# Kernel tuning notes

Hardware: AMD Instinct MI355X
Metric: run time of the kernel (lower is better)

## Reference

```python
import jax, jax.numpy as jnp
import numpy as np

N_NODES = 100000
N_EDGES = 1000000
N_GRAPHS = 16
D_NODE = 64
D_EDGE = 32
D_GLOB = 32
OUT_DIM = 64
IN1 = 2 * D_NODE + D_EDGE + D_GLOB  # 192
IN2 = D_NODE + OUT_DIM + D_GLOB     # 160


def setup_inputs() -> dict:
    key = jax.random.key(0)
    ks = jax.random.split(key, 9)
    x = jax.random.normal(ks[0], (N_NODES, D_NODE), dtype=jnp.float32)
    edge_index = jax.random.randint(ks[1], (2, N_EDGES), 0, N_NODES, dtype=jnp.int64 if jax.config.jax_enable_x64 else jnp.int32)
    edge_attr = jax.random.normal(ks[2], (N_EDGES, D_EDGE), dtype=jnp.float32)
    u = jax.random.normal(ks[3], (N_GRAPHS, D_GLOB), dtype=jnp.float32)
    batch = jnp.sort(jax.random.randint(ks[4], (N_NODES,), 0, N_GRAPHS))
    # Linear params (kaiming-ish scale)
    W1 = jax.random.normal(ks[5], (IN1, OUT_DIM), dtype=jnp.float32) / np.sqrt(IN1)
    b1 = jnp.zeros((OUT_DIM,), dtype=jnp.float32)
    W2 = jax.random.normal(ks[6], (IN2, OUT_DIM), dtype=jnp.float32) / np.sqrt(IN2)
    b2 = jnp.zeros((OUT_DIM,), dtype=jnp.float32)
    return {"x": x, "edge_index": edge_index, "edge_attr": edge_attr, "u": u,
            "batch": batch, "W1": W1, "b1": b1, "W2": W2, "b2": b2}


def reference(x, edge_index, edge_attr, u, batch, W1, b1, W2, b2):
    src = edge_index[0]  # [E]
    dst = edge_index[1]  # [E]
    u_per_node = u[batch]  # [N, Du] gather globals to nodes
    # gather-concat: [E, 2D + De + Du]
    all_feat = jnp.concatenate([x[dst], x[src], edge_attr, u_per_node[dst]], axis=-1)
    # mlp_1 + ReLU on every edge message
    msg = jax.nn.relu(all_feat @ W1 + b1)  # [E, out]
    # scatter-sum to destination nodes
    agg = jax.ops.segment_sum(msg, dst, num_segments=x.shape[0])  # [N, out]
    # mlp_2 + ReLU on nodes
    node_in = jnp.concatenate([x, agg, u_per_node], axis=-1)  # [N, D + out + Du]
    return jax.nn.relu(node_in @ W2 + b2)
```

## Files before the change

kernel.cpp:

```cpp
#include <hip/hip_runtime.h>

constexpr int N_NODES = 100000;
constexpr int N_EDGES = 1000000;
constexpr int D_NODE  = 64;
constexpr int D_EDGE  = 32;
constexpr int D_GLOB  = 32;
constexpr int OUT_DIM = 64;
constexpr int K1 = 2*D_NODE + D_EDGE + D_GLOB;
constexpr int K2 = D_NODE + OUT_DIM + D_GLOB;

typedef _Float16 f16x8 __attribute__((ext_vector_type(8)));
typedef unsigned short ushort8_t __attribute__((ext_vector_type(8)));
typedef float floatx16 __attribute__((ext_vector_type(16)));

constexpr int FS = 200;

constexpr size_t WS_W1T = 0;
constexpr size_t WS_W2T = 24576;
constexpr size_t WS_UB  = 45056;
constexpr size_t WS_XB  = 46080;

__device__ inline unsigned pack_f2(float a, float b) {
    auto h = __builtin_amdgcn_cvt_pkrtz(a, b);
    return __builtin_bit_cast(unsigned, h);
}

__global__ __launch_bounds__(256) void prep_kernel(
    const float* __restrict__ x, const float* __restrict__ u,
    const float* __restrict__ W1, const float* __restrict__ W2,
    unsigned short* __restrict__ ws_w1t, unsigned short* __restrict__ ws_w2t,
    unsigned short* __restrict__ ws_ub, unsigned short* __restrict__ ws_xb)
{
    const int t = blockIdx.x * 256 + threadIdx.x;
    const int stride = gridDim.x * 256;
    const float4* x4 = (const float4*)x;
    for (int i = t; i < N_NODES * 16; i += stride) {
        float4 v = x4[i];
        uint2 pk;
        pk.x = pack_f2(v.x, v.y);
        pk.y = pack_f2(v.z, v.w);
        *(uint2*)&ws_xb[i * 4] = pk;
    }
    for (int i = t; i < K1 * 64; i += stride) {
        int k = i >> 6, n = i & 63;
        _Float16 h = (_Float16)W1[i];
        ws_w1t[n * K1 + k] = __builtin_bit_cast(unsigned short, h);
    }
    for (int i = t; i < K2 * 64; i += stride) {
        int k = i >> 6, n = i & 63;
        _Float16 h = (_Float16)W2[i];
        ws_w2t[n * K2 + k] = __builtin_bit_cast(unsigned short, h);
    }
    for (int i = t; i < 16 * D_GLOB; i += stride) {
        _Float16 h = (_Float16)u[i];
        ws_ub[i] = __builtin_bit_cast(unsigned short, h);
    }
}

__global__ __launch_bounds__(256, 4) void edge_kernel(
    const unsigned short* __restrict__ xb, const int* __restrict__ ei,
    const float* __restrict__ ea, const unsigned short* __restrict__ ub,
    const int* __restrict__ batch, const unsigned short* __restrict__ W1t,
    const float* __restrict__ b1, float* __restrict__ out)
{
    __shared__ __align__(16) unsigned short smem[64 * FS];
    __shared__ int s_dst[64];
    __shared__ int s_src[64];
    __shared__ int s_b[64];

    const int tid  = threadIdx.x;
    const int lane = tid & 63;
    const int wv   = tid >> 6;
    const int tile = blockIdx.x;
    const int eh   = wv >> 1;
    const int nh   = wv & 1;
    const int col  = lane & 31;
    const int half = lane >> 5;

    if (tid < 64) {
        int e = tile * 64 + tid;
        int d = ei[N_EDGES + e];
        s_dst[tid] = d;
        s_src[tid] = ei[e];
        s_b[tid]   = batch[d];
    }

    f16x8 Wf[12];
    #pragma unroll
    for (int s = 0; s < 12; ++s)
        Wf[s] = __builtin_bit_cast(f16x8,
            *(const ushort8_t*)&W1t[(nh*32 + col) * K1 + s*16 + half*8]);

    const int chp = (lane & 31) * 2;
    const float2 bv = *(const float2*)&b1[chp];

    __syncthreads();

    const float4* ea4 = (const float4*)ea;
    for (int q = tid; q < 64 * 24; q += 256) {
        int el = q / 24;
        int c  = q - el * 24;
        uint4 pk;
        if (c < 8)       pk = *(const uint4*)&xb[s_dst[el] * 64 + c * 8];
        else if (c < 16) pk = *(const uint4*)&xb[s_src[el] * 64 + (c - 8) * 8];
        else if (c < 20) {
            float4 v0 = ea4[(tile*64 + el) * 8 + (c - 16) * 2 + 0];
            float4 v1 = ea4[(tile*64 + el) * 8 + (c - 16) * 2 + 1];
            pk.x = pack_f2(v0.x, v0.y); pk.y = pack_f2(v0.z, v0.w);
            pk.z = pack_f2(v1.x, v1.y); pk.w = pack_f2(v1.z, v1.w);
        } else           pk = *(const uint4*)&ub[s_b[el] * 32 + (c - 20) * 8];
        *(uint4*)&smem[el * FS + c * 8] = pk;
    }
    __syncthreads();

    floatx16 acc = {0,0,0,0,0,0,0,0,0,0,0,0,0,0,0,0};
    #pragma unroll
    for (int s = 0; s < 12; ++s) {
        f16x8 a = __builtin_bit_cast(f16x8,
            *(const ushort8_t*)&smem[(eh*32 + col) * FS + s*16 + half*8]);
        acc = __builtin_amdgcn_mfma_f32_32x32x16_f16(a, Wf[s], acc, 0, 0, 0);
    }

    __syncthreads();
    float* smemf = (float*)smem;
    #pragma unroll
    for (int r = 0; r < 16; ++r) {
        int e = eh*32 + (r & 3) + 8*(r >> 2) + 4*half;
        smemf[e * 64 + nh*32 + col] = acc[r];
    }
    __syncthreads();

    #pragma unroll
    for (int it = 0; it < 8; ++it) {
        int e = wv*16 + it*2 + half;
        float2 m = *(const float2*)&smemf[e * 64 + chp];
        float v0 = m.x + bv.x; v0 = v0 > 0.f ? v0 : 0.f;
        float v1 = m.y + bv.y; v1 = v1 > 0.f ? v1 : 0.f;
        unsigned pk = pack_f2(v0, v1);
        unsigned short* p = (unsigned short*)out + (size_t)s_dst[e] * 128 + chp;
        asm volatile("global_atomic_pk_add_f16 %0, %1, off"
                     :: "v"(p), "v"(pk) : "memory");
    }
}

__global__ __launch_bounds__(256, 4) void node_kernel(
    const unsigned short* __restrict__ xb, const unsigned short* __restrict__ ub,
    const int* __restrict__ batch, const unsigned short* __restrict__ W2t,
    const float* __restrict__ b2, float* __restrict__ out)
{
    __shared__ __align__(16) unsigned short smem[64 * FS];
    __shared__ int s_b[64];

    const int tid  = threadIdx.x;
    const int lane = tid & 63;
    const int wv   = tid >> 6;
    const int base = blockIdx.x * 64;
    const int eh   = wv >> 1;
    const int nh   = wv & 1;
    const int col  = lane & 31;
    const int half = lane >> 5;

    if (tid < 64) {
        int n = base + tid;
        s_b[tid] = (n < N_NODES) ? batch[n] : 0;
    }

    f16x8 Bf[10];
    #pragma unroll
    for (int s = 0; s < 10; ++s)
        Bf[s] = __builtin_bit_cast(f16x8,
            *(const ushort8_t*)&W2t[(nh*32 + col) * K2 + s*16 + half*8]);
    const float b2v = b2[nh*32 + col];

    __syncthreads();

    const unsigned short* aggb = (const unsigned short*)out;
    for (int q = tid; q < 64 * 20; q += 256) {
        int nl = q / 20;
        int c  = q - nl * 20;
        int n  = base + nl;
        uint4 pk;
        if (n >= N_NODES) pk = uint4{0, 0, 0, 0};
        else if (c < 8)   pk = *(const uint4*)&xb[n * 64 + c * 8];
        else if (c < 16)  pk = *(const uint4*)&aggb[(size_t)n * 128 + (c - 8) * 8];
        else              pk = *(const uint4*)&ub[s_b[nl] * 32 + (c - 16) * 8];
        *(uint4*)&smem[nl * FS + c * 8] = pk;
    }
    __syncthreads();

    floatx16 acc = {0,0,0,0,0,0,0,0,0,0,0,0,0,0,0,0};
    #pragma unroll
    for (int s = 0; s < 10; ++s) {
        f16x8 a = __builtin_bit_cast(f16x8,
            *(const ushort8_t*)&smem[(eh*32 + col) * FS + s*16 + half*8]);
        acc = __builtin_amdgcn_mfma_f32_32x32x16_f16(a, Bf[s], acc, 0, 0, 0);
    }

    #pragma unroll
    for (int r = 0; r < 16; ++r) {
        int n = base + eh*32 + (r & 3) + 8*(r >> 2) + 4*half;
        if (n < N_NODES) {
            float vv = acc[r] + b2v;
            out[n * 64 + nh*32 + col] = vv > 0.f ? vv : 0.f;
        }
    }
}

extern "C" void kernel_launch(void* const* d_in, const int* in_sizes, int n_in,
                              void* d_out, int out_size, void* d_ws, size_t ws_size,
                              hipStream_t stream) {
    const float* x     = (const float*)d_in[0];
    const int*   ei    = (const int*)d_in[1];
    const float* ea    = (const float*)d_in[2];
    const float* u     = (const float*)d_in[3];
    const int*   batch = (const int*)d_in[4];
    const float* W1    = (const float*)d_in[5];
    const float* b1    = (const float*)d_in[6];
    const float* W2    = (const float*)d_in[7];
    const float* b2    = (const float*)d_in[8];
    float* out = (float*)d_out;

    unsigned short* ws_w1t = (unsigned short*)((char*)d_ws + WS_W1T);
    unsigned short* ws_w2t = (unsigned short*)((char*)d_ws + WS_W2T);
    unsigned short* ws_ub  = (unsigned short*)((char*)d_ws + WS_UB);
    unsigned short* ws_xb  = (unsigned short*)((char*)d_ws + WS_XB);

    (void)hipMemsetAsync(out, 0, (size_t)out_size * sizeof(float), stream);

    prep_kernel<<<2048, 256, 0, stream>>>(x, u, W1, W2, ws_w1t, ws_w2t, ws_ub, ws_xb);
    edge_kernel<<<N_EDGES / 64, 256, 0, stream>>>(ws_xb, ei, ea, ws_ub, batch, ws_w1t, b1, out);
    node_kernel<<<(N_NODES + 63) / 64, 256, 0, stream>>>(ws_xb, ws_ub, batch, ws_w2t, b2, out);
}
```

Baseline: 437.3 us.

## Sort edges by destination and pre-reduce messages before atomic scatter

Adds a counting sort of edges by destination node (histogram, two-level prefix scan, atomic scatter into a permutation), and the edge kernel now processes edges in sorted order. Within each 16-edge run the epilogue accumulates consecutive same-destination messages in registers before issuing the packed f16 atomic, reducing atomic traffic. It also raises launch-bound occupancy hints to 6. The cost is extra kernels and passes over edge_index, plus gathers of edge_attr that are no longer contiguous. With about 10 edges per node on average, the runs of equal destinations inside 16-edge groups are short.

```diff
diff --git a/kernel.cpp b/kernel.cpp
--- a/kernel.cpp
+++ b/kernel.cpp
@@ -15,10 +15,14 @@
 
 constexpr int FS = 200;
 
-constexpr size_t WS_W1T = 0;
-constexpr size_t WS_W2T = 24576;
-constexpr size_t WS_UB  = 45056;
-constexpr size_t WS_XB  = 46080;
+constexpr size_t WS_W1T  = 0;
+constexpr size_t WS_W2T  = 24576;
+constexpr size_t WS_UB   = 45056;
+constexpr size_t WS_XB   = 46080;
+constexpr size_t WS_CNT  = 12846080;
+constexpr size_t WS_CUR  = 13370368;
+constexpr size_t WS_SORT = 13894656;
+constexpr int BSUM_BASE  = 130048;
 
 __device__ inline unsigned pack_f2(float a, float b) {
     auto h = __builtin_amdgcn_cvt_pkrtz(a, b);
@@ -28,6 +32,7 @@
 __global__ __launch_bounds__(256) void prep_kernel(
     const float* __restrict__ x, const float* __restrict__ u,
     const float* __restrict__ W1, const float* __restrict__ W2,
+    const int* __restrict__ ei, int* __restrict__ cnt,
     unsigned short* __restrict__ ws_w1t, unsigned short* __restrict__ ws_w2t,
     unsigned short* __restrict__ ws_ub, unsigned short* __restrict__ ws_xb)
 {
@@ -41,6 +46,8 @@
         pk.y = pack_f2(v.z, v.w);
         *(uint2*)&ws_xb[i * 4] = pk;
     }
+    for (int i = t; i < N_EDGES; i += stride)
+        atomicAdd(&cnt[ei[N_EDGES + i]], 1);
     for (int i = t; i < K1 * 64; i += stride) {
         int k = i >> 6, n = i & 63;
         _Float16 h = (_Float16)W1[i];
@@ -57,13 +64,71 @@
     }
 }
 
-__global__ __launch_bounds__(256, 4) void edge_kernel(
+__global__ __launch_bounds__(256) void scan_a_kernel(
+    const int* __restrict__ cnt, int* __restrict__ cursor, int* __restrict__ bsum)
+{
+    __shared__ int l[256];
+    const int t = threadIdx.x;
+    const int idx = blockIdx.x * 256 + t;
+    int4 v = ((const int4*)cnt)[idx];
+    int s = v.x + v.y + v.z + v.w;
+    l[t] = s;
+    __syncthreads();
+    for (int off = 1; off < 256; off <<= 1) {
+        int a = (t >= off) ? l[t - off] : 0;
+        __syncthreads();
+        l[t] += a;
+        __syncthreads();
+    }
+    int ex = l[t] - s;
+    int4 o;
+    o.x = ex; o.y = ex + v.x; o.z = o.y + v.y; o.w = o.z + v.z;
+    ((int4*)cursor)[idx] = o;
+    if (t == 255) bsum[blockIdx.x] = l[255];
+}
+
+__global__ __launch_bounds__(256) void scan_c_kernel(
+    const int* __restrict__ bsum, int* __restrict__ cursor)
+{
+    __shared__ int sb[128];
+    __shared__ int soff;
+    const int t = threadIdx.x;
+    if (t < 128) sb[t] = bsum[t];
+    __syncthreads();
+    if (t == 0) {
+        int s = 0;
+        for (int i = 0; i < (int)blockIdx.x; ++i) s += sb[i];
+        soff = s;
+    }
+    __syncthreads();
+    const int idx = blockIdx.x * 256 + t;
+    int4 v = ((const int4*)cursor)[idx];
+    v.x += soff; v.y += soff; v.z += soff; v.w += soff;
+    ((int4*)cursor)[idx] = v;
+}
+
+__global__ __launch_bounds__(256) void scatter_kernel(
+    const int* __restrict__ ei, int* __restrict__ cursor,
+    int* __restrict__ sorted_e)
+{
+    const int t = blockIdx.x * 256 + threadIdx.x;
+    const int stride = gridDim.x * 256;
+    for (int e = t; e < N_EDGES; e += stride) {
+        int d = ei[N_EDGES + e];
+        int pos = atomicAdd(&cursor[d], 1);
+        sorted_e[pos] = e;
+    }
+}
+
+__global__ __launch_bounds__(256, 6) void edge_kernel(
     const unsigned short* __restrict__ xb, const int* __restrict__ ei,
     const float* __restrict__ ea, const unsigned short* __restrict__ ub,
-    const int* __restrict__ batch, const unsigned short* __restrict__ W1t,
+    const int* __restrict__ batch, const int* __restrict__ sorted_e,
+    const unsigned short* __restrict__ W1t,
     const float* __restrict__ b1, float* __restrict__ out)
 {
     __shared__ __align__(16) unsigned short smem[64 * FS];
+    __shared__ int s_e[64];
     __shared__ int s_dst[64];
     __shared__ int s_src[64];
     __shared__ int s_b[64];
@@ -76,10 +141,12 @@
     const int nh   = wv & 1;
     const int col  = lane & 31;
     const int half = lane >> 5;
+    const float4* ea4 = (const float4*)ea;
 
     if (tid < 64) {
-        int e = tile * 64 + tid;
+        int e = sorted_e[tile * 64 + tid];
         int d = ei[N_EDGES + e];
+        s_e[tid]   = e;
         s_dst[tid] = d;
         s_src[tid] = ei[e];
         s_b[tid]   = batch[d];
@@ -96,16 +163,15 @@
 
     __syncthreads();
 
-    const float4* ea4 = (const float4*)ea;
     for (int q = tid; q < 64 * 24; q += 256) {
         int el = q / 24;
         int c  = q - el * 24;
         uint4 pk;
-        if (c < 8)       pk = *(const uint4*)&xb[s_dst[el] * 64 + c * 8];
-        else if (c < 16) pk = *(const uint4*)&xb[s_src[el] * 64 + (c - 8) * 8];
+        if (c < 8)       pk = *(const uint4*)&xb[(size_t)s_dst[el] * 64 + c * 8];
+        else if (c < 16) pk = *(const uint4*)&xb[(size_t)s_src[el] * 64 + (c - 8) * 8];
         else if (c < 20) {
-            float4 v0 = ea4[(tile*64 + el) * 8 + (c - 16) * 2 + 0];
-            float4 v1 = ea4[(tile*64 + el) * 8 + (c - 16) * 2 + 1];
+            float4 v0 = ea4[(size_t)s_e[el] * 8 + (c - 16) * 2 + 0];
+            float4 v1 = ea4[(size_t)s_e[el] * 8 + (c - 16) * 2 + 1];
             pk.x = pack_f2(v0.x, v0.y); pk.y = pack_f2(v0.z, v0.w);
             pk.z = pack_f2(v1.x, v1.y); pk.w = pack_f2(v1.z, v1.w);
         } else           pk = *(const uint4*)&ub[s_b[el] * 32 + (c - 20) * 8];
@@ -130,20 +196,32 @@
     }
     __syncthreads();
 
-    #pragma unroll
-    for (int it = 0; it < 8; ++it) {
-        int e = wv*16 + it*2 + half;
-        float2 m = *(const float2*)&smemf[e * 64 + chp];
-        float v0 = m.x + bv.x; v0 = v0 > 0.f ? v0 : 0.f;
-        float v1 = m.y + bv.y; v1 = v1 > 0.f ? v1 : 0.f;
-        unsigned pk = pack_f2(v0, v1);
-        unsigned short* p = (unsigned short*)out + (size_t)s_dst[e] * 128 + chp;
+    if (tid < 128) {
+        const int g = tid >> 5;
+        float r0 = 0.f, r1 = 0.f;
+        int cur = s_dst[g * 16];
+        for (int j = 0; j < 16; ++j) {
+            int ee = g * 16 + j;
+            int d = s_dst[ee];
+            if (d != cur) {
+                unsigned pk = pack_f2(r0, r1);
+                unsigned short* p = (unsigned short*)out + (size_t)cur * 128 + chp;
+                asm volatile("global_atomic_pk_add_f16 %0, %1, off"
+                             :: "v"(p), "v"(pk) : "memory");
+                r0 = 0.f; r1 = 0.f; cur = d;
+            }
+            float2 m = *(const float2*)&smemf[ee * 64 + chp];
+            float v0 = m.x + bv.x; r0 += (v0 > 0.f ? v0 : 0.f);
+            float v1 = m.y + bv.y; r1 += (v1 > 0.f ? v1 : 0.f);
+        }
+        unsigned pk = pack_f2(r0, r1);
+        unsigned short* p = (unsigned short*)out + (size_t)cur * 128 + chp;
         asm volatile("global_atomic_pk_add_f16 %0, %1, off"
                      :: "v"(p), "v"(pk) : "memory");
     }
 }
 
-__global__ __launch_bounds__(256, 4) void node_kernel(
+__global__ __launch_bounds__(256, 6) void node_kernel(
     const unsigned short* __restrict__ xb, const unsigned short* __restrict__ ub,
     const int* __restrict__ batch, const unsigned short* __restrict__ W2t,
     const float* __restrict__ b2, float* __restrict__ out)
@@ -181,7 +259,7 @@
         int n  = base + nl;
         uint4 pk;
         if (n >= N_NODES) pk = uint4{0, 0, 0, 0};
-        else if (c < 8)   pk = *(const uint4*)&xb[n * 64 + c * 8];
+        else if (c < 8)   pk = *(const uint4*)&xb[(size_t)n * 64 + c * 8];
         else if (c < 16)  pk = *(const uint4*)&aggb[(size_t)n * 128 + (c - 8) * 8];
         else              pk = *(const uint4*)&ub[s_b[nl] * 32 + (c - 16) * 8];
         *(uint4*)&smem[nl * FS + c * 8] = pk;
@@ -201,7 +279,7 @@
         int n = base + eh*32 + (r & 3) + 8*(r >> 2) + 4*half;
         if (n < N_NODES) {
             float vv = acc[r] + b2v;
-            out[n * 64 + nh*32 + col] = vv > 0.f ? vv : 0.f;
+            out[(size_t)n * 64 + nh*32 + col] = vv > 0.f ? vv : 0.f;
         }
     }
 }
@@ -224,10 +302,21 @@
     unsigned short* ws_w2t = (unsigned short*)((char*)d_ws + WS_W2T);
     unsigned short* ws_ub  = (unsigned short*)((char*)d_ws + WS_UB);
     unsigned short* ws_xb  = (unsigned short*)((char*)d_ws + WS_XB);
+    int* cnt    = (int*)((char*)d_ws + WS_CNT);
+    int* cursor = (int*)((char*)d_ws + WS_CUR);
+    int* sorted = (int*)((char*)d_ws + WS_SORT);
+    int* bsum   = cnt + BSUM_BASE;
 
     (void)hipMemsetAsync(out, 0, (size_t)out_size * sizeof(float), stream);
-
-    prep_kernel<<<2048, 256, 0, stream>>>(x, u, W1, W2, ws_w1t, ws_w2t, ws_ub, ws_xb);
-    edge_kernel<<<N_EDGES / 64, 256, 0, stream>>>(ws_xb, ei, ea, ws_ub, batch, ws_w1t, b1, out);
-    node_kernel<<<(N_NODES + 63) / 64, 256, 0, stream>>>(ws_xb, ws_ub, batch, ws_w2t, b2, out);
-}
+    (void)hipMemsetAsync(cnt, 0, 524288, stream);
+
+    prep_kernel<<<2048, 256, 0, stream>>>(x, u, W1, W2, ei, cnt,
+                                          ws_w1t, ws_w2t, ws_ub, ws_xb);
+    scan_a_kernel<<<128, 256, 0, stream>>>(cnt, cursor, bsum);
+    scan_c_kernel<<<128, 256, 0, stream>>>(bsum, cursor);
+    scatter_kernel<<<2048, 256, 0, stream>>>(ei, cursor, sorted);
+    edge_kernel<<<N_EDGES / 64, 256, 0, stream>>>(ws_xb, ei, ea, ws_ub, batch,
+                                                  sorted, ws_w1t, b1, out);
+    node_kernel<<<(N_NODES + 63) / 64, 256, 0, stream>>>(ws_xb, ws_ub, batch,
+                                                         ws_w2t, b2, out);
+}
```

Measured after the change: 560.4 us. 28.1% more time.
